# Optimization experiments

Hardware: AMD Instinct MI355X
Metric: run time of the kernel (lower is better)

## Reference

```python
import jax, jax.numpy as jnp
import numpy as np
from jax.scipy.special import logsumexp

HEADS = 8
BUCKETS = 64
DIM = 64
TEMPERATURE = 0.7
SINKHORN_ITER = 8
EPS = 1e-06


def setup_inputs() -> dict:
    key = jax.random.key(0)
    k1, k2, k3, k4, k5 = jax.random.split(key, 5)
    bh, seq = 32, 8192
    q = jax.random.normal(k1, (bh, seq, DIM), dtype=jnp.float32)
    k = jax.random.normal(k2, (bh, seq, DIM), dtype=jnp.float32)
    q_pos_emb = jax.random.normal(k3, (1, HEADS, BUCKETS, DIM), dtype=jnp.float32)
    k_pos_emb = jax.random.normal(k4, (1, HEADS, BUCKETS, DIM), dtype=jnp.float32)
    # gumbel noise: -log(-log(u)) with the module's eps, same shape as R
    u = jax.random.uniform(k5, (bh, BUCKETS, BUCKETS), dtype=jnp.float32)
    gumbel = -jnp.log(-jnp.log(u + EPS) + EPS)
    return {"q": q, "k": k, "q_pos_emb": q_pos_emb, "k_pos_emb": k_pos_emb, "gumbel": gumbel}


def _expand_merge(pos, b):
    # (1, heads, buckets, dim) -> (b*heads, buckets, dim)
    _, h, bu, d = pos.shape
    return jnp.broadcast_to(pos, (b, h, bu, d)).reshape(b * h, bu, d)


def reference(q, k, q_pos_emb, k_pos_emb, gumbel):
    bh, seq, d = q.shape
    b = bh // HEADS
    # bucket + mean over bucket contents: (bh, buckets, seq//buckets, d) -> (bh, buckets, d)
    b_q = q.reshape(bh, BUCKETS, -1, d).mean(axis=2)
    b_k = k.reshape(bh, BUCKETS, -1, d).mean(axis=2)
    sq = b_q + _expand_merge(q_pos_emb, b)
    sk = b_k + _expand_merge(k_pos_emb, b)
    R = jnp.einsum('bie,bje->bij', sq, sk)  # (bh, buckets, buckets)
    # gumbel_sinkhorn(relu(R))
    r = jnp.log(jax.nn.relu(R) + EPS)
    r = (r + gumbel) / TEMPERATURE

    def step(r, _):
        r = r - logsumexp(r, axis=2, keepdims=True)
        r = r - logsumexp(r, axis=1, keepdims=True)
        return r, None

    r, _ = jax.lax.scan(step, r, None, length=SINKHORN_ITER)
    return jnp.exp(r)
```

## Files before the change

kernel.cpp:

```cpp
#include <hip/hip_runtime.h>
#include <math.h>

#define HEADS 8
#define BUCKETS 64
#define DIM 64
#define SEQ 8192
#define BH 32
#define ROWS_PER_BUCKET (SEQ / BUCKETS)
#define EPS 1e-6f
#define LOG2E 1.4426950408889634f
#define INV_T (1.0f / 0.7f)
#define SINKHORN_ITER_COUNT 8

static __device__ __forceinline__ float fast_exp2(float x) {
#if __has_builtin(__builtin_amdgcn_exp2f)
    return __builtin_amdgcn_exp2f(x);
#else
    return exp2f(x);
#endif
}
static __device__ __forceinline__ float fast_log2(float x) {
#if __has_builtin(__builtin_amdgcn_logf)
    return __builtin_amdgcn_logf(x);
#else
    return log2f(x);
#endif
}

__global__ __launch_bounds__(256) void bucket_mean_kernel(
    const float* __restrict__ q, const float* __restrict__ k,
    const float* __restrict__ q_pos, const float* __restrict__ k_pos,
    float* __restrict__ sq, float* __restrict__ sk) {

    const int which = blockIdx.y;
    const int bh = blockIdx.x >> 6;
    const int bucket = blockIdx.x & 63;
    const float* __restrict__ src = which ? k : q;
    const float* __restrict__ pos = which ? k_pos : q_pos;
    float* __restrict__ dst = which ? sk : sq;

    const int t = threadIdx.x;
    const int c = t & 15;
    const int rg = t >> 4;

    const float4* __restrict__ src4 = (const float4*)src;
    size_t base = ((size_t)bh * SEQ + (size_t)bucket * ROWS_PER_BUCKET + (size_t)rg * 8) * (DIM / 4) + c;

    float4 acc = make_float4(0.f, 0.f, 0.f, 0.f);
#pragma unroll
    for (int rr = 0; rr < 8; ++rr) {
        float4 v = src4[base + (size_t)rr * (DIM / 4)];
        acc.x += v.x; acc.y += v.y; acc.z += v.z; acc.w += v.w;
    }

    __shared__ float4 sm[16][16];
    sm[rg][c] = acc;
    __syncthreads();
#pragma unroll
    for (int s = 8; s > 0; s >>= 1) {
        if (rg < s) {
            float4 o = sm[rg + s][c];
            float4 m = sm[rg][c];
            m.x += o.x; m.y += o.y; m.z += o.z; m.w += o.w;
            sm[rg][c] = m;
        }
        __syncthreads();
    }

    if (rg == 0) {
        const int head = bh & (HEADS - 1);
        float4 p = ((const float4*)pos)[(head * BUCKETS + bucket) * (DIM / 4) + c];
        float4 m = sm[0][c];
        const float inv = 1.0f / (float)ROWS_PER_BUCKET;
        float4 r;
        r.x = m.x * inv + p.x; r.y = m.y * inv + p.y;
        r.z = m.z * inv + p.z; r.w = m.w * inv + p.w;
        ((float4*)dst)[(bh * BUCKETS + bucket) * (DIM / 4) + c] = r;
    }
}

__global__ __launch_bounds__(1024) void sinkhorn_kernel(
    const float* __restrict__ sq, const float* __restrict__ sk,
    const float* __restrict__ gumbel, float* __restrict__ out) {

    const int bh = blockIdx.x;
    const int t = threadIdx.x;
    const int lane = t & 63;
    const int w = t >> 6;

    __shared__ float sq_s[64][64];
    __shared__ float sk_s[64][65];
    __shared__ float r_s[64][65];

    {
        const float4* __restrict__ sq4 = (const float4*)(sq + bh * 4096);
        const float4* __restrict__ sk4 = (const float4*)(sk + bh * 4096);
        int row = t >> 4, ch = t & 15;
        float4 v = sq4[t];
        *(float4*)&sq_s[row][ch * 4] = v;
        float4 u = sk4[t];
        sk_s[row][ch * 4 + 0] = u.x; sk_s[row][ch * 4 + 1] = u.y;
        sk_s[row][ch * 4 + 2] = u.z; sk_s[row][ch * 4 + 3] = u.w;
    }
    __syncthreads();

    float acc[4];
#pragma unroll
    for (int ii = 0; ii < 4; ++ii) acc[ii] = 0.f;
    for (int d = 0; d < 64; ++d) {
        float skv = sk_s[lane][d];
#pragma unroll
        for (int ii = 0; ii < 4; ++ii)
            acc[ii] = fmaf(sq_s[w * 4 + ii][d], skv, acc[ii]);
    }

    const float* __restrict__ g = gumbel + bh * 4096;
#pragma unroll
    for (int ii = 0; ii < 4; ++ii) {
        int i = w * 4 + ii;
        float Rp = fmaxf(acc[ii], 0.f) + EPS;
        float y = (fast_log2(Rp) + g[i * 64 + lane] * LOG2E) * INV_T;
        r_s[i][lane] = y;
    }
    __syncthreads();

    for (int it = 0; it < SINKHORN_ITER_COUNT; ++it) {
#pragma unroll
        for (int ii = 0; ii < 4; ++ii) {
            int i = w * 4 + ii;
            float x = r_s[i][lane];
            float s = fast_exp2(x);
#pragma unroll
            for (int off = 32; off > 0; off >>= 1) s += __shfl_xor(s, off);
            r_s[i][lane] = x - fast_log2(s);
        }
        __syncthreads();
#pragma unroll
        for (int jj = 0; jj < 4; ++jj) {
            int jc = w * 4 + jj;
            float x = r_s[lane][jc];
            float s = fast_exp2(x);
#pragma unroll
            for (int off = 32; off > 0; off >>= 1) s += __shfl_xor(s, off);
            r_s[lane][jc] = x - fast_log2(s);
        }
        __syncthreads();
    }

    float* __restrict__ o = out + bh * 4096;
#pragma unroll
    for (int ii = 0; ii < 4; ++ii) {
        int i = w * 4 + ii;
        o[i * 64 + lane] = fast_exp2(r_s[i][lane]);
    }
}

extern "C" void kernel_launch(void* const* d_in, const int* in_sizes, int n_in,
                              void* d_out, int out_size, void* d_ws, size_t ws_size,
                              hipStream_t stream) {
    const float* q   = (const float*)d_in[0];
    const float* k   = (const float*)d_in[1];
    const float* qpe = (const float*)d_in[2];
    const float* kpe = (const float*)d_in[3];
    const float* gum = (const float*)d_in[4];
    float* out = (float*)d_out;

    float* sq = (float*)d_ws;
    float* sk = sq + BH * BUCKETS * DIM;

    bucket_mean_kernel<<<dim3(BH * BUCKETS, 2), 256, 0, stream>>>(q, k, qpe, kpe, sq, sk);
    sinkhorn_kernel<<<BH, 1024, 0, stream>>>(sq, sk, gum, out);
}
```

Baseline: 49.27 us.

## Assign one wavefront per bucket and reduce with shuffles instead of shared memory

```diff
diff --git a/kernel.cpp b/kernel.cpp
--- a/kernel.cpp
+++ b/kernel.cpp
@@ -32,51 +32,46 @@
     const float* __restrict__ q_pos, const float* __restrict__ k_pos,
     float* __restrict__ sq, float* __restrict__ sk) {
 
-    const int which = blockIdx.y;
-    const int bh = blockIdx.x >> 6;
-    const int bucket = blockIdx.x & 63;
+    const int lane = threadIdx.x & 63;
+    const int task = blockIdx.x * 4 + (threadIdx.x >> 6);
+    const int which = task >> 11;
+    const int bh = (task >> 6) & 31;
+    const int bucket = task & 63;
+
     const float* __restrict__ src = which ? k : q;
     const float* __restrict__ pos = which ? k_pos : q_pos;
     float* __restrict__ dst = which ? sk : sq;
 
-    const int t = threadIdx.x;
-    const int c = t & 15;
-    const int rg = t >> 4;
+    const int c = lane & 15;
+    const int rs = lane >> 4;
 
-    const float4* __restrict__ src4 = (const float4*)src;
-    size_t base = ((size_t)bh * SEQ + (size_t)bucket * ROWS_PER_BUCKET + (size_t)rg * 8) * (DIM / 4) + c;
+    const float4* __restrict__ s4 = (const float4*)(src
+        + ((size_t)bh * SEQ + (size_t)bucket * ROWS_PER_BUCKET) * DIM);
 
     float4 acc = make_float4(0.f, 0.f, 0.f, 0.f);
 #pragma unroll
-    for (int rr = 0; rr < 8; ++rr) {
-        float4 v = src4[base + (size_t)rr * (DIM / 4)];
+    for (int i = 0; i < 32; ++i) {
+        float4 v = s4[(size_t)(i * 4 + rs) * (DIM / 4) + c];
         acc.x += v.x; acc.y += v.y; acc.z += v.z; acc.w += v.w;
     }
 
-    __shared__ float4 sm[16][16];
-    sm[rg][c] = acc;
-    __syncthreads();
 #pragma unroll
-    for (int s = 8; s > 0; s >>= 1) {
-        if (rg < s) {
-            float4 o = sm[rg + s][c];
-            float4 m = sm[rg][c];
-            m.x += o.x; m.y += o.y; m.z += o.z; m.w += o.w;
-            sm[rg][c] = m;
-        }
-        __syncthreads();
+    for (int off = 16; off <= 32; off <<= 1) {
+        acc.x += __shfl_xor(acc.x, off);
+        acc.y += __shfl_xor(acc.y, off);
+        acc.z += __shfl_xor(acc.z, off);
+        acc.w += __shfl_xor(acc.w, off);
     }
 
-    if (rg == 0) {
-        const int head = bh & (HEADS - 1);
-        float4 p = ((const float4*)pos)[(head * BUCKETS + bucket) * (DIM / 4) + c];
-        float4 m = sm[0][c];
-        const float inv = 1.0f / (float)ROWS_PER_BUCKET;
-        float4 r;
-        r.x = m.x * inv + p.x; r.y = m.y * inv + p.y;
-        r.z = m.z * inv + p.z; r.w = m.w * inv + p.w;
+    const int head = bh & (HEADS - 1);
+    float4 p = ((const float4*)pos)[(head * BUCKETS + bucket) * (DIM / 4) + c];
+    const float inv = 1.0f / (float)ROWS_PER_BUCKET;
+    float4 r;
+    r.x = acc.x * inv + p.x; r.y = acc.y * inv + p.y;
+    r.z = acc.z * inv + p.z; r.w = acc.w * inv + p.w;
+
+    if (lane < 16)
         ((float4*)dst)[(bh * BUCKETS + bucket) * (DIM / 4) + c] = r;
-    }
 }
 
 __global__ __launch_bounds__(1024) void sinkhorn_kernel(
@@ -168,6 +163,6 @@
     float* sq = (float*)d_ws;
     float* sk = sq + BH * BUCKETS * DIM;
 
-    bucket_mean_kernel<<<dim3(BH * BUCKETS, 2), 256, 0, stream>>>(q, k, qpe, kpe, sq, sk);
+    bucket_mean_kernel<<<1024, 256, 0, stream>>>(q, k, qpe, kpe, sq, sk);
     sinkhorn_kernel<<<BH, 1024, 0, stream>>>(sq, sk, gum, out);
 }
```

After: 49.28 us. Within noise of the previous version (+0.0%).
